# Kernel tuning notes

Measured on AMD Instinct MI355X. Metric: run time of the kernel, lower is better.

## Reference

```python
import jax, jax.numpy as jnp
import numpy as np


def setup_inputs() -> dict:
    key = jax.random.key(0)
    k1, k2, k3, k4 = jax.random.split(key, 4)
    B, N, F, H, O = 4, 2048, 256, 8, 256
    nodes = jax.random.normal(k1, (B, N, F), dtype=jnp.float32)
    W_heads = jax.random.normal(k2, (H, F, F), dtype=jnp.float32) * (1.0 / np.sqrt(F))
    W_out = jax.random.normal(k3, (H * F, O), dtype=jnp.float32) * (1.0 / np.sqrt(H * F))
    bias = jax.random.normal(k4, (O,), dtype=jnp.float32) * 0.02
    return {"nodes": nodes, "W_heads": W_heads, "W_out": W_out, "bias": bias}


def reference(nodes, W_heads, W_out, bias):
    # nodes: [B,N,F]; W_heads: [H,F,F]; W_out: [H*F,O]; bias: [O]
    B, N, F = nodes.shape
    H = W_heads.shape[0]
    norm = 1.0 / jnp.sqrt(jnp.asarray(F, dtype=nodes.dtype))
    # per-head bilinear scores: (x @ W_h) @ x^T  -> [B,H,N,N]
    xw = jnp.einsum('bnf,hfg->bhng', nodes, W_heads)
    scores = jnp.einsum('bhng,bmg->bhnm', xw, nodes) * norm
    att = jax.nn.softmax(scores, axis=-1)
    # messages: att @ x (V = input nodes) -> [B,H,N,F]
    msgs = jnp.einsum('bhnm,bmf->bhnf', att, nodes)
    # concat heads along feature axis (head 0 first) -> [B,N,H*F]
    msgs = msgs.transpose(0, 2, 1, 3).reshape(B, N, H * F)
    return jnp.matmul(msgs, W_out) + bias
```

## Files before the change

### kernel.cpp

```cpp
#include <hip/hip_runtime.h>
#include <hip/hip_bf16.h>

#define B_ 4
#define N_ 2048
#define F_ 256
#define H_ 8
#define O_ 256

#define SCALE_QK 0.09016844005556021f

typedef __attribute__((ext_vector_type(8))) short short8;
typedef __attribute__((ext_vector_type(4))) short s16x4;
typedef __attribute__((ext_vector_type(4))) float f32x4;
typedef __attribute__((ext_vector_type(4))) unsigned int u32x4;

static __device__ __forceinline__ float bf2f(short u) {
    unsigned int x = ((unsigned int)(unsigned short)u) << 16;
    return __builtin_bit_cast(float, x);
}
static __device__ __forceinline__ short f2bf(float f) {
    unsigned int x = __builtin_bit_cast(unsigned int, f);
    unsigned int lsb = (x >> 16) & 1u;
    x += 0x7fffu + lsb;
    return (short)(x >> 16);
}
static __device__ __forceinline__ unsigned int cvtpk(float a, float b) {
    unsigned int r;
    asm("v_cvt_pk_bf16_f32 %0, %1, %2" : "=v"(r) : "v"(a), "v"(b));
    return r;
}

static __device__ __forceinline__ void gld16(const short* g, short* l) {
    __builtin_amdgcn_global_load_lds(
        (const __attribute__((address_space(1))) void*)g,
        (__attribute__((address_space(3))) void*)l, 16, 0, 0);
}

__global__ __launch_bounds__(256) void cvtT_kernel(const float* __restrict__ src,
                                                   short* __restrict__ dstT,
                                                   short* __restrict__ dst2,
                                                   int R, int C) {
    __shared__ short tile[32][33];
    src  += (size_t)blockIdx.z * R * C;
    dstT += (size_t)blockIdx.z * R * C;
    if (dst2) dst2 += (size_t)blockIdx.z * R * C;
    int tx = threadIdx.x, ty = threadIdx.y;
    int c0 = blockIdx.x * 32, r0 = blockIdx.y * 32;
#pragma unroll
    for (int j = 0; j < 4; j++) {
        int r = r0 + ty + j * 8;
        short v = f2bf(src[(size_t)r * C + c0 + tx]);
        tile[ty + j * 8][tx] = v;
        if (dst2) dst2[(size_t)r * C + c0 + tx] = v;
    }
    __syncthreads();
#pragma unroll
    for (int j = 0; j < 4; j++) {
        int c = c0 + ty + j * 8;
        dstT[(size_t)c * R + r0 + tx] = tile[tx][ty + j * 8];
    }
}

__global__ __launch_bounds__(512) void out_kernel(const short* __restrict__ msgs,
                                                  const short* __restrict__ WoutT,
                                                  const float* __restrict__ bias,
                                                  float* __restrict__ out) {
    __shared__ short sA[2][64 * 64];
    __shared__ short sB[2][128 * 64];
    int mt = blockIdx.x, nt = blockIdx.y;
    int tid = threadIdx.x, w = tid >> 6, l = tid & 63, lq = l & 15, quad = l >> 4;
    const short* Arow = msgs  + (size_t)(mt * 64)  * (H_ * F_);
    const short* Brow = WoutT + (size_t)(nt * 128) * (H_ * F_);
    int xk = (l & 7) ^ (l >> 3);

    f32x4 acc[4];
#pragma unroll
    for (int i = 0; i < 4; i++) acc[i] = (f32x4)(0.f);

#define STAGE_OUT(KB, BI) do {                                               \
        gld16(&Arow[(size_t)(w * 8 + (l >> 3)) * (H_ * F_) + (KB) * 64 + xk * 8], \
              &sA[BI][w * 8 * 64]);                                          \
        gld16(&Brow[(size_t)(w * 16 + (l >> 3)) * (H_ * F_) + (KB) * 64 + xk * 8], \
              &sB[BI][w * 16 * 64]);                                         \
        gld16(&Brow[(size_t)(w * 16 + 8 + (l >> 3)) * (H_ * F_) + (KB) * 64 + xk * 8], \
              &sB[BI][(w * 16 + 8) * 64]);                                   \
    } while (0)

    STAGE_OUT(0, 0);
    __syncthreads();

#pragma unroll 1
    for (int kb = 0; kb < 32; kb++) {
        int cur = kb & 1;
        if (kb < 31) STAGE_OUT(kb + 1, cur ^ 1);
        int arow = (w & 3) * 16 + lq;
#pragma unroll
        for (int kk = 0; kk < 2; kk++) {
            short8 af = *(const short8*)&sA[cur][arow * 64 + (((kk * 4 + quad) ^ (arow & 7)) * 8)];
#pragma unroll
            for (int ct = 0; ct < 4; ct++) {
                int brow = (w >> 2) * 64 + ct * 16 + lq;
                short8 bf = *(const short8*)&sB[cur][brow * 64 + (((kk * 4 + quad) ^ (brow & 7)) * 8)];
                acc[ct] = __builtin_amdgcn_mfma_f32_16x16x32_bf16(af, bf, acc[ct], 0, 0, 0);
            }
        }
        __syncthreads();
    }

#pragma unroll
    for (int ct = 0; ct < 4; ct++) {
        int gcol = nt * 128 + (w >> 2) * 64 + ct * 16 + lq;
        float bv = bias[gcol];
#pragma unroll
        for (int r = 0; r < 4; r++) {
            int row = mt * 64 + (w & 3) * 16 + quad * 4 + r;
            out[(size_t)row * O_ + gcol] = acc[ct][r] + bv;
        }
    }
}


#define STAGE_KV(KT, KVF, KVTF) do {                                         \
    _Pragma("unroll")                                                        \
    for (int i_ = 0; i_ < 4; i_++) {                                         \
        int rk_ = w * 8 + i_ * 2 + (l >> 5);                                 \
        int bk_ = (l & 31) ^ (rk_ & 31);                                     \
        gld16(&Xb[(size_t)((KT) * 64 + rk_) * F_ + bk_ * 8],                 \
              &KVF[(w * 8 + i_ * 2) * 256]);                                 \
        int rt_ = w * 32 + i_ * 8 + (l >> 3);                                \
        int bt_ = (l & 7) ^ (rt_ & 7);                                       \
        gld16(&XTb[(size_t)rt_ * N_ + (KT) * 64 + bt_ * 8],                  \
              &KVTF[(w * 32 + i_ * 8) * 64]);                                \
    }                                                                        \
} while (0)

#define COMPUTE_KT(KVF, KVTF) do {                                           \
    f32x4 sacc[4];                                                           \
    _Pragma("unroll")                                                        \
    for (int ct = 0; ct < 4; ct++) sacc[ct] = (f32x4)(0.f);                  \
    __builtin_amdgcn_s_setprio(1);                                           \
    _Pragma("unroll")                                                        \
    for (int kk = 0; kk < 8; kk++) {                                         \
        _Pragma("unroll")                                                    \
        for (int ct = 0; ct < 4; ct++) {                                     \
            int arow = ct * 16 + lq;                                         \
            int ab = (kk * 4 + quad) ^ (arow & 31);                          \
            short8 af = *(const short8*)&KVF[arow * 256 + ab * 8];           \
            sacc[ct] = __builtin_amdgcn_mfma_f32_16x16x32_bf16(af, aq[kk], sacc[ct], 0, 0, 0); \
        }                                                                    \
    }                                                                        \
    __builtin_amdgcn_s_setprio(0);                                           \
    float mx = -INFINITY;                                                    \
    _Pragma("unroll")                                                        \
    for (int ct = 0; ct < 4; ct++)                                           \
        _Pragma("unroll")                                                    \
        for (int r_ = 0; r_ < 4; r_++) mx = fmaxf(mx, sacc[ct][r_]);         \
    mx = fmaxf(mx, __shfl_xor(mx, 16));                                      \
    mx = fmaxf(mx, __shfl_xor(mx, 32));                                      \
    if (!__all(mx - m_q <= 8.0f)) {                \
        float mn = fmaxf(m_q, mx);                                           \
        float alpha = exp2f(m_q - mn);                                       \
        m_q = mn;                                                            \
        l_q *= alpha;                                                        \
        _Pragma("unroll")                                                    \
        for (int ct = 0; ct < 16; ct++)                                      \
            _Pragma("unroll")                                                \
            for (int r_ = 0; r_ < 4; r_++) oacc[ct][r_] *= alpha;            \
    }                                                                        \
    float pv[4][4]; float s_ = 0.f;                                          \
    _Pragma("unroll")                                                        \
    for (int ct = 0; ct < 4; ct++)                                           \
        _Pragma("unroll")                                                    \
        for (int r_ = 0; r_ < 4; r_++) {                                     \
            pv[ct][r_] = exp2f(sacc[ct][r_] - m_q);                          \
            s_ += pv[ct][r_];                                                \
        }                                                                    \
    s_ += __shfl_xor(s_, 16);                                                \
    s_ += __shfl_xor(s_, 32);                                                \
    l_q += s_;                                                               \
    unsigned int w2[4][2];                                                   \
    _Pragma("unroll")                                                        \
    for (int ct = 0; ct < 4; ct++) {                                         \
        w2[ct][0] = cvtpk(pv[ct][0], pv[ct][1]);                             \
        w2[ct][1] = cvtpk(pv[ct][2], pv[ct][3]);                             \
    }                                                                        \
    int sl0 = (2 * (quad & 1)) * 16 + lq;                                    \
    int sl1 = sl0 + 16;                                                      \
    bool hi = (quad >> 1) != 0;                                              \
    short8 pfrag[2];                                                         \
    _Pragma("unroll")                                                        \
    for (int kk = 0; kk < 2; kk++) {                                         \
        unsigned int u0 = __shfl((int)w2[2 * kk][0], sl0);                   \
        unsigned int u1 = __shfl((int)w2[2 * kk][1], sl0);                   \
        unsigned int u2 = __shfl((int)w2[2 * kk][0], sl1);                   \
        unsigned int u3 = __shfl((int)w2[2 * kk][1], sl1);                   \
        unsigned int v0 = __shfl((int)w2[2 * kk + 1][0], sl0);               \
        unsigned int v1 = __shfl((int)w2[2 * kk + 1][1], sl0);               \
        unsigned int v2 = __shfl((int)w2[2 * kk + 1][0], sl1);               \
        unsigned int v3 = __shfl((int)w2[2 * kk + 1][1], sl1);               \
        u32x4 pk = { hi ? v0 : u0, hi ? v1 : u1, hi ? v2 : u2, hi ? v3 : u3 }; \
        pfrag[kk] = __builtin_bit_cast(short8, pk);                          \
    }                                                                        \
    __builtin_amdgcn_s_setprio(1);                                           \
    _Pragma("unroll")                                                        \
    for (int ct = 0; ct < 16; ct++) {                                        \
        int arow = ct * 16 + lq;                                             \
        short8 a0 = *(const short8*)&KVTF[arow * 64 + ((quad) ^ (arow & 7)) * 8]; \
        short8 a1 = *(const short8*)&KVTF[arow * 64 + ((4 + quad) ^ (arow & 7)) * 8]; \
        oacc[ct] = __builtin_amdgcn_mfma_f32_16x16x32_bf16(a0, pfrag[0], oacc[ct], 0, 0, 0); \
        oacc[ct] = __builtin_amdgcn_mfma_f32_16x16x32_bf16(a1, pfrag[1], oacc[ct], 0, 0, 0); \
    }                                                                        \
    __builtin_amdgcn_s_setprio(0);                                           \
} while (0)

__global__ __launch_bounds__(512) void attn_kernel(const short* __restrict__ X,
                                                   const short* __restrict__ WhT,
                                                   const short* __restrict__ XT,
                                                   short* __restrict__ msgs) {
    __shared__ short kvfA[64 * 256];
    __shared__ short kvfB[64 * 256];
    __shared__ short kvTfA[256 * 64];
    __shared__ short kvTfB[256 * 64];

    int qt = blockIdx.x, bh = blockIdx.y, b = bh >> 3, h = bh & 7;
    int tid = threadIdx.x, w = tid >> 6, l = tid & 63, lq = l & 15, quad = l >> 4;
    int q0 = qt * 128;

    const short* Xb  = X  + (size_t)b * N_ * F_;
    const short* XTb = XT + (size_t)b * F_ * N_;
    const short* Whh = WhT + (size_t)h * F_ * F_;

    f32x4 oacc[16];
    short8 aq[8];

#pragma unroll
    for (int i = 0; i < 16; i++) oacc[i] = (f32x4)(0.f);
    {
        short* xdst = (w < 4) ? kvfA : kvfB;
        int wl = w & 3;
#pragma unroll
        for (int i = 0; i < 8; i++) {
            int r = wl * 16 + i * 2 + (l >> 5);
            int bb = (l & 31) ^ (r & 31);
            gld16(&Xb[(size_t)(q0 + ((w >> 2) * 64) + r) * F_ + bb * 8],
                  &xdst[(wl * 16 + i * 2) * 256]);
        }
    }
    const short* xsrc = (w < 4) ? kvfA : kvfB;
#pragma unroll 1
    for (int kb = 0; kb < 4; kb++) {
        __syncthreads();
#pragma unroll
        for (int i = 0; i < 4; i++) {
            int rt = w * 32 + i * 8 + (l >> 3);
            int bt = (l & 7) ^ (rt & 7);
            gld16(&Whh[(size_t)rt * F_ + kb * 64 + bt * 8], &kvTfA[(w * 32 + i * 8) * 64]);
        }
        __syncthreads();
#pragma unroll
        for (int kk = 0; kk < 2; kk++) {
            int arow = (w & 3) * 16 + lq;
            int ab = (kb * 8 + kk * 4 + quad) ^ (arow & 31);
            short8 af = *(const short8*)&xsrc[arow * 256 + ab * 8];
#pragma unroll
            for (int ct = 0; ct < 16; ct++) {
                int brow = ct * 16 + lq;
                int bb = (kk * 4 + quad) ^ (brow & 7);
                short8 bf = *(const short8*)&kvTfA[brow * 64 + bb * 8];
                oacc[ct] = __builtin_amdgcn_mfma_f32_16x16x32_bf16(af, bf, oacc[ct], 0, 0, 0);
            }
        }
    }
    __syncthreads();
    {
        short* qdst = (w < 4) ? kvTfA : kvTfB;
#pragma unroll
        for (int ct = 0; ct < 16; ct++) {
#pragma unroll
            for (int r = 0; r < 4; r++) {
                int row = (w & 3) * 16 + quad * 4 + r;
                int col = ct * 16 + lq;
                int pb = (col >> 3) ^ (row & 31);
                qdst[row * 256 + pb * 8 + (col & 7)] = f2bf(oacc[ct][r] * SCALE_QK);
            }
        }
        __syncthreads();
#pragma unroll
        for (int kk = 0; kk < 8; kk++) {
            int row = (w & 3) * 16 + lq;
            int ab = (kk * 4 + quad) ^ (row & 31);
            aq[kk] = *(const short8*)&qdst[row * 256 + ab * 8];
        }
    }
    __syncthreads();

#pragma unroll
    for (int i = 0; i < 16; i++) oacc[i] = (f32x4)(0.f);
    float m_q = -INFINITY, l_q = 0.f;

    STAGE_KV(0, kvfA, kvTfA);
    __syncthreads();

#pragma unroll 1
    for (int kt2 = 0; kt2 < 16; kt2++) {
        STAGE_KV(2 * kt2 + 1, kvfB, kvTfB);
        COMPUTE_KT(kvfA, kvTfA);
        __syncthreads();
        STAGE_KV((2 * kt2 + 2) & 31, kvfA, kvTfA);
        COMPUTE_KT(kvfB, kvTfB);
        __syncthreads();
    }

    float inv = 1.f / l_q;
    short* Mout = msgs + (size_t)(b * N_ + q0 + w * 16 + lq) * (H_ * F_) + h * F_;
#pragma unroll
    for (int ct = 0; ct < 16; ct++) {
        s16x4 v4 = { f2bf(oacc[ct][0] * inv), f2bf(oacc[ct][1] * inv),
                     f2bf(oacc[ct][2] * inv), f2bf(oacc[ct][3] * inv) };
        *(s16x4*)&Mout[ct * 16 + quad * 4] = v4;
    }
}

extern "C" void kernel_launch(void* const* d_in, const int* in_sizes, int n_in,
                              void* d_out, int out_size, void* d_ws, size_t ws_size,
                              hipStream_t stream) {
    const float* nodes = (const float*)d_in[0];
    const float* Wh    = (const float*)d_in[1];
    const float* Wout  = (const float*)d_in[2];
    const float* bias  = (const float*)d_in[3];
    float* out = (float*)d_out;

    char* ws = (char*)d_ws;
    short* msgs   = (short*)(ws);
    short* WhT    = (short*)(ws + 33554432);
    short* WoutT  = (short*)(ws + 34603008);
    short* XT     = (short*)(ws + 35651584);
    short* Xbf    = (short*)(ws + 39845888);

    dim3 tblk(32, 8, 1);
    hipLaunchKernelGGL(cvtT_kernel, dim3(8, 8, 8),  tblk, 0, stream, Wh,    WhT,   (short*)nullptr, 256,  256);
    hipLaunchKernelGGL(cvtT_kernel, dim3(8, 64, 1), tblk, 0, stream, Wout,  WoutT, (short*)nullptr, 2048, 256);
    hipLaunchKernelGGL(cvtT_kernel, dim3(8, 64, 4), tblk, 0, stream, nodes, XT,    Xbf,             2048, 256);

    hipLaunchKernelGGL(attn_kernel, dim3(16, 32), dim3(512), 0, stream, Xbf, WhT, XT, msgs);
    hipLaunchKernelGGL(out_kernel,  dim3(128, 2), dim3(512), 0, stream, msgs, WoutT, bias, out);
}
```

Measured before the change: 289.0 us.

## Split KV tile across wave pairs, each wave handling two query blocks

Restructures the attention loop so each pair of waves shares 32 query rows. Each wave computes scores for two 16-row query blocks but only against half of each 64-key tile, reusing every K and V fragment loaded from LDS for two MFMAs. Partial softmax states (max and sum) and output accumulators are merged through shared memory at the end. This cuts LDS reads per MFMA and doubles the output accumulator registers, at the cost of a final cross-wave reduction and possibly lower occupancy.

```diff
diff --git a/kernel.cpp b/kernel.cpp
--- a/kernel.cpp
+++ b/kernel.cpp
@@ -135,80 +135,85 @@
 } while (0)
 
 #define COMPUTE_KT(KVF, KVTF) do {                                           \
-    f32x4 sacc[4];                                                           \
-    _Pragma("unroll")                                                        \
-    for (int ct = 0; ct < 4; ct++) sacc[ct] = (f32x4)(0.f);                  \
+    f32x4 sacc[2][2];                                                        \
+    _Pragma("unroll")                                                        \
+    for (int qb = 0; qb < 2; qb++)                                           \
+        _Pragma("unroll")                                                    \
+        for (int ct = 0; ct < 2; ct++) sacc[qb][ct] = (f32x4)(0.f);          \
     __builtin_amdgcn_s_setprio(1);                                           \
     _Pragma("unroll")                                                        \
     for (int kk = 0; kk < 8; kk++) {                                         \
         _Pragma("unroll")                                                    \
-        for (int ct = 0; ct < 4; ct++) {                                     \
-            int arow = ct * 16 + lq;                                         \
+        for (int ct = 0; ct < 2; ct++) {                                     \
+            int arow = KH + ct * 16 + lq;                                    \
             int ab = (kk * 4 + quad) ^ (arow & 31);                          \
             short8 af = *(const short8*)&KVF[arow * 256 + ab * 8];           \
-            sacc[ct] = __builtin_amdgcn_mfma_f32_16x16x32_bf16(af, aq[kk], sacc[ct], 0, 0, 0); \
+            sacc[0][ct] = __builtin_amdgcn_mfma_f32_16x16x32_bf16(af, aq[0][kk], sacc[0][ct], 0, 0, 0); \
+            sacc[1][ct] = __builtin_amdgcn_mfma_f32_16x16x32_bf16(af, aq[1][kk], sacc[1][ct], 0, 0, 0); \
         }                                                                    \
     }                                                                        \
     __builtin_amdgcn_s_setprio(0);                                           \
-    float mx = -INFINITY;                                                    \
-    _Pragma("unroll")                                                        \
-    for (int ct = 0; ct < 4; ct++)                                           \
-        _Pragma("unroll")                                                    \
-        for (int r_ = 0; r_ < 4; r_++) mx = fmaxf(mx, sacc[ct][r_]);         \
-    mx = fmaxf(mx, __shfl_xor(mx, 16));                                      \
-    mx = fmaxf(mx, __shfl_xor(mx, 32));                                      \
-    if (!__all(mx - m_q <= 8.0f)) {                \
-        float mn = fmaxf(m_q, mx);                                           \
-        float alpha = exp2f(m_q - mn);                                       \
-        m_q = mn;                                                            \
-        l_q *= alpha;                                                        \
-        _Pragma("unroll")                                                    \
-        for (int ct = 0; ct < 16; ct++)                                      \
+    unsigned int w2[2][2][2];                                                \
+    _Pragma("unroll")                                                        \
+    for (int qb = 0; qb < 2; qb++) {                                         \
+        float mx = -INFINITY;                                                \
+        _Pragma("unroll")                                                    \
+        for (int ct = 0; ct < 2; ct++)                                       \
             _Pragma("unroll")                                                \
-            for (int r_ = 0; r_ < 4; r_++) oacc[ct][r_] *= alpha;            \
-    }                                                                        \
-    float pv[4][4]; float s_ = 0.f;                                          \
-    _Pragma("unroll")                                                        \
-    for (int ct = 0; ct < 4; ct++)                                           \
-        _Pragma("unroll")                                                    \
-        for (int r_ = 0; r_ < 4; r_++) {                                     \
-            pv[ct][r_] = exp2f(sacc[ct][r_] - m_q);                          \
-            s_ += pv[ct][r_];                                                \
+            for (int r_ = 0; r_ < 4; r_++) mx = fmaxf(mx, sacc[qb][ct][r_]); \
+        mx = fmaxf(mx, __shfl_xor(mx, 16));                                  \
+        mx = fmaxf(mx, __shfl_xor(mx, 32));                                  \
+        if (!__all(mx - m_q[qb] <= 8.0f)) {               \
+            float mn = fmaxf(m_q[qb], mx);                                   \
+            float alpha = exp2f(m_q[qb] - mn);                               \
+            m_q[qb] = mn;                                                    \
+            l_q[qb] *= alpha;                                                \
+            _Pragma("unroll")                                                \
+            for (int ct = 0; ct < 16; ct++)                                  \
+                _Pragma("unroll")                                            \
+                for (int r_ = 0; r_ < 4; r_++) oacc[qb][ct][r_] *= alpha;    \
         }                                                                    \
-    s_ += __shfl_xor(s_, 16);                                                \
-    s_ += __shfl_xor(s_, 32);                                                \
-    l_q += s_;                                                               \
-    unsigned int w2[4][2];                                                   \
-    _Pragma("unroll")                                                        \
-    for (int ct = 0; ct < 4; ct++) {                                         \
-        w2[ct][0] = cvtpk(pv[ct][0], pv[ct][1]);                             \
-        w2[ct][1] = cvtpk(pv[ct][2], pv[ct][3]);                             \
+        float pv[2][4]; float s_ = 0.f;                                      \
+        _Pragma("unroll")                                                    \
+        for (int ct = 0; ct < 2; ct++)                                       \
+            _Pragma("unroll")                                                \
+            for (int r_ = 0; r_ < 4; r_++) {                                 \
+                pv[ct][r_] = exp2f(sacc[qb][ct][r_] - m_q[qb]);              \
+                s_ += pv[ct][r_];                                            \
+            }                                                                \
+        s_ += __shfl_xor(s_, 16);                                            \
+        s_ += __shfl_xor(s_, 32);                                            \
+        l_q[qb] += s_;                                                       \
+        _Pragma("unroll")                                                    \
+        for (int ct = 0; ct < 2; ct++) {                                     \
+            w2[qb][ct][0] = cvtpk(pv[ct][0], pv[ct][1]);                     \
+            w2[qb][ct][1] = cvtpk(pv[ct][2], pv[ct][3]);                     \
+        }                                                                    \
     }                                                                        \
     int sl0 = (2 * (quad & 1)) * 16 + lq;                                    \
     int sl1 = sl0 + 16;                                                      \
     bool hi = (quad >> 1) != 0;                                              \
     short8 pfrag[2];                                                         \
     _Pragma("unroll")                                                        \
-    for (int kk = 0; kk < 2; kk++) {                                         \
-        unsigned int u0 = __shfl((int)w2[2 * kk][0], sl0);                   \
-        unsigned int u1 = __shfl((int)w2[2 * kk][1], sl0);                   \
-        unsigned int u2 = __shfl((int)w2[2 * kk][0], sl1);                   \
-        unsigned int u3 = __shfl((int)w2[2 * kk][1], sl1);                   \
-        unsigned int v0 = __shfl((int)w2[2 * kk + 1][0], sl0);               \
-        unsigned int v1 = __shfl((int)w2[2 * kk + 1][1], sl0);               \
-        unsigned int v2 = __shfl((int)w2[2 * kk + 1][0], sl1);               \
-        unsigned int v3 = __shfl((int)w2[2 * kk + 1][1], sl1);               \
+    for (int qb = 0; qb < 2; qb++) {                                         \
+        unsigned int u0 = __shfl((int)w2[qb][0][0], sl0);                    \
+        unsigned int u1 = __shfl((int)w2[qb][0][1], sl0);                    \
+        unsigned int u2 = __shfl((int)w2[qb][0][0], sl1);                    \
+        unsigned int u3 = __shfl((int)w2[qb][0][1], sl1);                    \
+        unsigned int v0 = __shfl((int)w2[qb][1][0], sl0);                    \
+        unsigned int v1 = __shfl((int)w2[qb][1][1], sl0);                    \
+        unsigned int v2 = __shfl((int)w2[qb][1][0], sl1);                    \
+        unsigned int v3 = __shfl((int)w2[qb][1][1], sl1);                    \
         u32x4 pk = { hi ? v0 : u0, hi ? v1 : u1, hi ? v2 : u2, hi ? v3 : u3 }; \
-        pfrag[kk] = __builtin_bit_cast(short8, pk);                          \
+        pfrag[qb] = __builtin_bit_cast(short8, pk);                          \
     }                                                                        \
     __builtin_amdgcn_s_setprio(1);                                           \
     _Pragma("unroll")                                                        \
     for (int ct = 0; ct < 16; ct++) {                                        \
         int arow = ct * 16 + lq;                                             \
-        short8 a0 = *(const short8*)&KVTF[arow * 64 + ((quad) ^ (arow & 7)) * 8]; \
-        short8 a1 = *(const short8*)&KVTF[arow * 64 + ((4 + quad) ^ (arow & 7)) * 8]; \
-        oacc[ct] = __builtin_amdgcn_mfma_f32_16x16x32_bf16(a0, pfrag[0], oacc[ct], 0, 0, 0); \
-        oacc[ct] = __builtin_amdgcn_mfma_f32_16x16x32_bf16(a1, pfrag[1], oacc[ct], 0, 0, 0); \
+        short8 a0 = *(const short8*)&KVTF[arow * 64 + (((KH4 + quad) ^ (arow & 7)) * 8)]; \
+        oacc[0][ct] = __builtin_amdgcn_mfma_f32_16x16x32_bf16(a0, pfrag[0], oacc[0][ct], 0, 0, 0); \
+        oacc[1][ct] = __builtin_amdgcn_mfma_f32_16x16x32_bf16(a0, pfrag[1], oacc[1][ct], 0, 0, 0); \
     }                                                                        \
     __builtin_amdgcn_s_setprio(0);                                           \
 } while (0)
@@ -217,24 +222,27 @@
                                                    const short* __restrict__ WhT,
                                                    const short* __restrict__ XT,
                                                    short* __restrict__ msgs) {
-    __shared__ short kvfA[64 * 256];
-    __shared__ short kvfB[64 * 256];
-    __shared__ short kvTfA[256 * 64];
-    __shared__ short kvTfB[256 * 64];
+    __shared__ __attribute__((aligned(16))) short kvfA[64 * 256];
+    __shared__ __attribute__((aligned(16))) short kvfB[64 * 256];
+    __shared__ __attribute__((aligned(16))) short kvTfA[256 * 64];
+    __shared__ __attribute__((aligned(16))) short kvTfB[256 * 64];
+    __shared__ float mbuf[8][2][16];
+    __shared__ float lbuf[8][2][16];
 
     int qt = blockIdx.x, bh = blockIdx.y, b = bh >> 3, h = bh & 7;
     int tid = threadIdx.x, w = tid >> 6, l = tid & 63, lq = l & 15, quad = l >> 4;
     int q0 = qt * 128;
+    int KH = (w & 1) * 32, KH4 = (w & 1) * 4;
 
     const short* Xb  = X  + (size_t)b * N_ * F_;
     const short* XTb = XT + (size_t)b * F_ * N_;
     const short* Whh = WhT + (size_t)h * F_ * F_;
 
-    f32x4 oacc[16];
-    short8 aq[8];
-
-#pragma unroll
-    for (int i = 0; i < 16; i++) oacc[i] = (f32x4)(0.f);
+    f32x4 oacc[2][16];
+    short8 aq[2][8];
+
+#pragma unroll
+    for (int i = 0; i < 16; i++) oacc[0][i] = (f32x4)(0.f);
     {
         short* xdst = (w < 4) ? kvfA : kvfB;
         int wl = w & 3;
@@ -267,7 +275,7 @@
                 int brow = ct * 16 + lq;
                 int bb = (kk * 4 + quad) ^ (brow & 7);
                 short8 bf = *(const short8*)&kvTfA[brow * 64 + bb * 8];
-                oacc[ct] = __builtin_amdgcn_mfma_f32_16x16x32_bf16(af, bf, oacc[ct], 0, 0, 0);
+                oacc[0][ct] = __builtin_amdgcn_mfma_f32_16x16x32_bf16(af, bf, oacc[0][ct], 0, 0, 0);
             }
         }
     }
@@ -281,22 +289,28 @@
                 int row = (w & 3) * 16 + quad * 4 + r;
                 int col = ct * 16 + lq;
                 int pb = (col >> 3) ^ (row & 31);
-                qdst[row * 256 + pb * 8 + (col & 7)] = f2bf(oacc[ct][r] * SCALE_QK);
-            }
-        }
-        __syncthreads();
-#pragma unroll
-        for (int kk = 0; kk < 8; kk++) {
-            int row = (w & 3) * 16 + lq;
-            int ab = (kk * 4 + quad) ^ (row & 31);
-            aq[kk] = *(const short8*)&qdst[row * 256 + ab * 8];
-        }
-    }
-    __syncthreads();
-
-#pragma unroll
-    for (int i = 0; i < 16; i++) oacc[i] = (f32x4)(0.f);
-    float m_q = -INFINITY, l_q = 0.f;
+                qdst[row * 256 + pb * 8 + (col & 7)] = f2bf(oacc[0][ct][r] * SCALE_QK);
+            }
+        }
+        __syncthreads();
+        const short* qsrc = (w < 4) ? kvTfA : kvTfB;
+#pragma unroll
+        for (int qb = 0; qb < 2; qb++) {
+#pragma unroll
+            for (int kk = 0; kk < 8; kk++) {
+                int row = ((w >> 1) & 1) * 32 + qb * 16 + lq;
+                int ab = (kk * 4 + quad) ^ (row & 31);
+                aq[qb][kk] = *(const short8*)&qsrc[row * 256 + ab * 8];
+            }
+        }
+    }
+    __syncthreads();
+
+#pragma unroll
+    for (int qb = 0; qb < 2; qb++)
+#pragma unroll
+        for (int i = 0; i < 16; i++) oacc[qb][i] = (f32x4)(0.f);
+    float m_q[2] = { -INFINITY, -INFINITY }, l_q[2] = { 0.f, 0.f };
 
     STAGE_KV(0, kvfA, kvTfA);
     __syncthreads();
@@ -311,13 +325,50 @@
         __syncthreads();
     }
 
-    float inv = 1.f / l_q;
-    short* Mout = msgs + (size_t)(b * N_ + q0 + w * 16 + lq) * (H_ * F_) + h * F_;
-#pragma unroll
-    for (int ct = 0; ct < 16; ct++) {
-        s16x4 v4 = { f2bf(oacc[ct][0] * inv), f2bf(oacc[ct][1] * inv),
-                     f2bf(oacc[ct][2] * inv), f2bf(oacc[ct][3] * inv) };
-        *(s16x4*)&Mout[ct * 16 + quad * 4] = v4;
+#pragma unroll
+    for (int qb = 0; qb < 2; qb++) {
+        mbuf[w][qb][lq] = m_q[qb];
+        lbuf[w][qb][lq] = l_q[qb];
+    }
+    __syncthreads();
+    float a_own[2], inv[2];
+#pragma unroll
+    for (int qb = 0; qb < 2; qb++) {
+        float mp = mbuf[w ^ 1][qb][lq], lp = lbuf[w ^ 1][qb][lq];
+        float mm = fmaxf(m_q[qb], mp);
+        float ao = exp2f(m_q[qb] - mm), ap = exp2f(mp - mm);
+        a_own[qb] = ao;
+        inv[qb] = 1.f / (l_q[qb] * ao + lp * ap);
+    }
+    int pr = w >> 1;
+    float* obuf = (float*)(pr == 0 ? (void*)kvfA : pr == 1 ? (void*)kvfB
+                           : pr == 2 ? (void*)kvTfA : (void*)kvTfB);
+    if (!(w & 1)) {
+#pragma unroll
+        for (int qb = 0; qb < 2; qb++)
+#pragma unroll
+            for (int ct = 0; ct < 16; ct++) {
+                int word = (qb * 16 + lq) * 256 + ((ct * 16 + quad * 4) ^ ((lq & 7) * 4));
+                f32x4 v = oacc[qb][ct] * a_own[qb];
+                *(f32x4*)&obuf[word] = v;
+            }
+    }
+    __syncthreads();
+    if (w & 1) {
+        short* Mout = msgs + (size_t)(b * N_ + q0 + pr * 32 + lq) * (H_ * F_) + h * F_;
+#pragma unroll
+        for (int qb = 0; qb < 2; qb++) {
+#pragma unroll
+            for (int ct = 0; ct < 16; ct++) {
+                int word = (qb * 16 + lq) * 256 + ((ct * 16 + quad * 4) ^ ((lq & 7) * 4));
+                f32x4 o = *(const f32x4*)&obuf[word];
+                s16x4 v4;
+#pragma unroll
+                for (int r = 0; r < 4; r++)
+                    v4[r] = f2bf((o[r] + oacc[qb][ct][r] * a_own[qb]) * inv[qb]);
+                *(s16x4*)&Mout[(size_t)qb * 16 * (H_ * F_) + ct * 16 + quad * 4] = v4;
+            }
+        }
     }
 }
 
```

After: 454.0 us. 57.1% more time.

## Merge conversion launches and double-buffer W_head tiles in attention projection

Applied to the files above, without the earlier changes.

Folds the three transpose/convert launches into a single prep kernel that dispatches on block index, removing two kernel launches. In the attention kernel's Q-projection loop, the next W_head k-slice is now prefetched into an alternate LDS buffer while MFMAs run on the current one, replacing two barriers per iteration with one. Correctness depends on kvTfB being free during this phase, since it is reused later.

```diff
diff --git a/kernel.cpp b/kernel.cpp
--- a/kernel.cpp
+++ b/kernel.cpp
@@ -36,16 +36,33 @@
         (__attribute__((address_space(3))) void*)l, 16, 0, 0);
 }
 
-__global__ __launch_bounds__(256) void cvtT_kernel(const float* __restrict__ src,
-                                                   short* __restrict__ dstT,
-                                                   short* __restrict__ dst2,
-                                                   int R, int C) {
+__global__ __launch_bounds__(256) void prep_kernel(const float* __restrict__ nodes,
+                                                   const float* __restrict__ Wh,
+                                                   const float* __restrict__ Wout,
+                                                   short* __restrict__ Xbf,
+                                                   short* __restrict__ XT,
+                                                   short* __restrict__ WhT,
+                                                   short* __restrict__ WoutT) {
     __shared__ short tile[32][33];
-    src  += (size_t)blockIdx.z * R * C;
-    dstT += (size_t)blockIdx.z * R * C;
-    if (dst2) dst2 += (size_t)blockIdx.z * R * C;
+    int id = blockIdx.x;
+    const float* src; short* dstT; short* dst2; int R, C, bx, by;
+    if (id < 512) {
+        int z = id >> 6, rem = id & 63;
+        src = Wh + (size_t)z * 65536; dstT = WhT + (size_t)z * 65536; dst2 = nullptr;
+        R = 256; C = 256; bx = rem & 7; by = rem >> 3;
+    } else if (id < 1024) {
+        int rem = id - 512;
+        src = Wout; dstT = WoutT; dst2 = nullptr;
+        R = 2048; C = 256; bx = rem & 7; by = rem >> 3;
+    } else {
+        int rem = id - 1024;
+        int z = rem >> 9; rem &= 511;
+        src = nodes + (size_t)z * 524288; dstT = XT + (size_t)z * 524288;
+        dst2 = Xbf + (size_t)z * 524288;
+        R = 2048; C = 256; bx = rem & 7; by = rem >> 3;
+    }
     int tx = threadIdx.x, ty = threadIdx.y;
-    int c0 = blockIdx.x * 32, r0 = blockIdx.y * 32;
+    int c0 = bx * 32, r0 = by * 32;
 #pragma unroll
     for (int j = 0; j < 4; j++) {
         int r = r0 + ty + j * 8;
@@ -246,17 +263,29 @@
                   &xdst[(wl * 16 + i * 2) * 256]);
         }
     }
-    const short* xsrc = (w < 4) ? kvfA : kvfB;
-#pragma unroll 1
-    for (int kb = 0; kb < 4; kb++) {
-        __syncthreads();
+    {
 #pragma unroll
         for (int i = 0; i < 4; i++) {
             int rt = w * 32 + i * 8 + (l >> 3);
             int bt = (l & 7) ^ (rt & 7);
-            gld16(&Whh[(size_t)rt * F_ + kb * 64 + bt * 8], &kvTfA[(w * 32 + i * 8) * 64]);
-        }
-        __syncthreads();
+            gld16(&Whh[(size_t)rt * F_ + bt * 8], &kvTfA[(w * 32 + i * 8) * 64]);
+        }
+    }
+    const short* xsrc = (w < 4) ? kvfA : kvfB;
+    __syncthreads();
+#pragma unroll 1
+    for (int kb = 0; kb < 4; kb++) {
+        short* wnext = (kb & 1) ? kvTfA : kvTfB;
+        const short* wsrc = (kb & 1) ? kvTfB : kvTfA;
+        if (kb < 3) {
+#pragma unroll
+            for (int i = 0; i < 4; i++) {
+                int rt = w * 32 + i * 8 + (l >> 3);
+                int bt = (l & 7) ^ (rt & 7);
+                gld16(&Whh[(size_t)rt * F_ + (kb + 1) * 64 + bt * 8],
+                      &wnext[(w * 32 + i * 8) * 64]);
+            }
+        }
 #pragma unroll
         for (int kk = 0; kk < 2; kk++) {
             int arow = (w & 3) * 16 + lq;
@@ -266,12 +295,12 @@
             for (int ct = 0; ct < 16; ct++) {
                 int brow = ct * 16 + lq;
                 int bb = (kk * 4 + quad) ^ (brow & 7);
-                short8 bf = *(const short8*)&kvTfA[brow * 64 + bb * 8];
+                short8 bf = *(const short8*)&wsrc[brow * 64 + bb * 8];
                 oacc[ct] = __builtin_amdgcn_mfma_f32_16x16x32_bf16(af, bf, oacc[ct], 0, 0, 0);
             }
         }
-    }
-    __syncthreads();
+        __syncthreads();
+    }
     {
         short* qdst = (w < 4) ? kvTfA : kvTfB;
 #pragma unroll
@@ -337,11 +366,8 @@
     short* XT     = (short*)(ws + 35651584);
     short* Xbf    = (short*)(ws + 39845888);
 
-    dim3 tblk(32, 8, 1);
-    hipLaunchKernelGGL(cvtT_kernel, dim3(8, 8, 8),  tblk, 0, stream, Wh,    WhT,   (short*)nullptr, 256,  256);
-    hipLaunchKernelGGL(cvtT_kernel, dim3(8, 64, 1), tblk, 0, stream, Wout,  WoutT, (short*)nullptr, 2048, 256);
-    hipLaunchKernelGGL(cvtT_kernel, dim3(8, 64, 4), tblk, 0, stream, nodes, XT,    Xbf,             2048, 256);
-
+    hipLaunchKernelGGL(prep_kernel, dim3(3072), dim3(32, 8), 0, stream,
+                       nodes, Wh, Wout, Xbf, XT, WhT, WoutT);
     hipLaunchKernelGGL(attn_kernel, dim3(16, 32), dim3(512), 0, stream, Xbf, WhT, XT, msgs);
     hipLaunchKernelGGL(out_kernel,  dim3(128, 2), dim3(512), 0, stream, msgs, WoutT, bias, out);
 }
```

Measured after the change: 294.9 us. +2.1%, slower.

## Process two query groups per wave in attention kernel with 4-wave blocks

Applied to the files above, without the earlier changes.

Each attention block now runs 4 waves instead of 8, and each wave handles two 16-row query groups. Every K/V fragment read from LDS feeds two MFMAs, which halves LDS read traffic per unit of math. The cost is roughly double the accumulator registers per wave (two 16-tile output accumulators plus two query fragment sets) and fewer waves per block to hide latency. Launch bounds are set to one block per SM-equivalent so the compiler can use more registers.

```diff
diff --git a/kernel.cpp b/kernel.cpp
--- a/kernel.cpp
+++ b/kernel.cpp
@@ -122,22 +122,24 @@
 
 #define STAGE_KV(KT, KVF, KVTF) do {                                         \
     _Pragma("unroll")                                                        \
-    for (int i_ = 0; i_ < 4; i_++) {                                         \
-        int rk_ = w * 8 + i_ * 2 + (l >> 5);                                 \
+    for (int i_ = 0; i_ < 8; i_++) {                                         \
+        int rk_ = w * 16 + i_ * 2 + (l >> 5);                                \
         int bk_ = (l & 31) ^ (rk_ & 31);                                     \
         gld16(&Xb[(size_t)((KT) * 64 + rk_) * F_ + bk_ * 8],                 \
-              &KVF[(w * 8 + i_ * 2) * 256]);                                 \
-        int rt_ = w * 32 + i_ * 8 + (l >> 3);                                \
+              &KVF[(w * 16 + i_ * 2) * 256]);                                \
+        int rt_ = w * 64 + i_ * 8 + (l >> 3);                                \
         int bt_ = (l & 7) ^ (rt_ & 7);                                       \
         gld16(&XTb[(size_t)rt_ * N_ + (KT) * 64 + bt_ * 8],                  \
-              &KVTF[(w * 32 + i_ * 8) * 64]);                                \
+              &KVTF[(w * 64 + i_ * 8) * 64]);                                \
     }                                                                        \
 } while (0)
 
 #define COMPUTE_KT(KVF, KVTF) do {                                           \
-    f32x4 sacc[4];                                                           \
-    _Pragma("unroll")                                                        \
-    for (int ct = 0; ct < 4; ct++) sacc[ct] = (f32x4)(0.f);                  \
+    f32x4 sacc[2][4];                                                        \
+    _Pragma("unroll")                                                        \
+    for (int qg = 0; qg < 2; qg++)                                           \
+        _Pragma("unroll")                                                    \
+        for (int ct = 0; ct < 4; ct++) sacc[qg][ct] = (f32x4)(0.f);          \
     __builtin_amdgcn_s_setprio(1);                                           \
     _Pragma("unroll")                                                        \
     for (int kk = 0; kk < 8; kk++) {                                         \
@@ -146,60 +148,64 @@
             int arow = ct * 16 + lq;                                         \
             int ab = (kk * 4 + quad) ^ (arow & 31);                          \
             short8 af = *(const short8*)&KVF[arow * 256 + ab * 8];           \
-            sacc[ct] = __builtin_amdgcn_mfma_f32_16x16x32_bf16(af, aq[kk], sacc[ct], 0, 0, 0); \
+            sacc[0][ct] = __builtin_amdgcn_mfma_f32_16x16x32_bf16(af, aq[0][kk], sacc[0][ct], 0, 0, 0); \
+            sacc[1][ct] = __builtin_amdgcn_mfma_f32_16x16x32_bf16(af, aq[1][kk], sacc[1][ct], 0, 0, 0); \
         }                                                                    \
     }                                                                        \
     __builtin_amdgcn_s_setprio(0);                                           \
-    float mx = -INFINITY;                                                    \
-    _Pragma("unroll")                                                        \
-    for (int ct = 0; ct < 4; ct++)                                           \
-        _Pragma("unroll")                                                    \
-        for (int r_ = 0; r_ < 4; r_++) mx = fmaxf(mx, sacc[ct][r_]);         \
-    mx = fmaxf(mx, __shfl_xor(mx, 16));                                      \
-    mx = fmaxf(mx, __shfl_xor(mx, 32));                                      \
-    if (!__all(mx - m_q <= 8.0f)) {                \
-        float mn = fmaxf(m_q, mx);                                           \
-        float alpha = exp2f(m_q - mn);                                       \
-        m_q = mn;                                                            \
-        l_q *= alpha;                                                        \
-        _Pragma("unroll")                                                    \
-        for (int ct = 0; ct < 16; ct++)                                      \
-            _Pragma("unroll")                                                \
-            for (int r_ = 0; r_ < 4; r_++) oacc[ct][r_] *= alpha;            \
-    }                                                                        \
-    float pv[4][4]; float s_ = 0.f;                                          \
-    _Pragma("unroll")                                                        \
-    for (int ct = 0; ct < 4; ct++)                                           \
-        _Pragma("unroll")                                                    \
-        for (int r_ = 0; r_ < 4; r_++) {                                     \
-            pv[ct][r_] = exp2f(sacc[ct][r_] - m_q);                          \
-            s_ += pv[ct][r_];                                                \
-        }                                                                    \
-    s_ += __shfl_xor(s_, 16);                                                \
-    s_ += __shfl_xor(s_, 32);                                                \
-    l_q += s_;                                                               \
-    unsigned int w2[4][2];                                                   \
-    _Pragma("unroll")                                                        \
-    for (int ct = 0; ct < 4; ct++) {                                         \
-        w2[ct][0] = cvtpk(pv[ct][0], pv[ct][1]);                             \
-        w2[ct][1] = cvtpk(pv[ct][2], pv[ct][3]);                             \
-    }                                                                        \
+    short8 pfrag[2][2];                                                      \
     int sl0 = (2 * (quad & 1)) * 16 + lq;                                    \
     int sl1 = sl0 + 16;                                                      \
     bool hi = (quad >> 1) != 0;                                              \
-    short8 pfrag[2];                                                         \
-    _Pragma("unroll")                                                        \
-    for (int kk = 0; kk < 2; kk++) {                                         \
-        unsigned int u0 = __shfl((int)w2[2 * kk][0], sl0);                   \
-        unsigned int u1 = __shfl((int)w2[2 * kk][1], sl0);                   \
-        unsigned int u2 = __shfl((int)w2[2 * kk][0], sl1);                   \
-        unsigned int u3 = __shfl((int)w2[2 * kk][1], sl1);                   \
-        unsigned int v0 = __shfl((int)w2[2 * kk + 1][0], sl0);               \
-        unsigned int v1 = __shfl((int)w2[2 * kk + 1][1], sl0);               \
-        unsigned int v2 = __shfl((int)w2[2 * kk + 1][0], sl1);               \
-        unsigned int v3 = __shfl((int)w2[2 * kk + 1][1], sl1);               \
-        u32x4 pk = { hi ? v0 : u0, hi ? v1 : u1, hi ? v2 : u2, hi ? v3 : u3 }; \
-        pfrag[kk] = __builtin_bit_cast(short8, pk);                          \
+    _Pragma("unroll")                                                        \
+    for (int qg = 0; qg < 2; qg++) {                                         \
+        float mx = -INFINITY;                                                \
+        _Pragma("unroll")                                                    \
+        for (int ct = 0; ct < 4; ct++)                                       \
+            _Pragma("unroll")                                                \
+            for (int r_ = 0; r_ < 4; r_++) mx = fmaxf(mx, sacc[qg][ct][r_]); \
+        mx = fmaxf(mx, __shfl_xor(mx, 16));                                  \
+        mx = fmaxf(mx, __shfl_xor(mx, 32));                                  \
+        if (!__all(mx - m_q[qg] <= 8.0f)) {        \
+            float mn = fmaxf(m_q[qg], mx);                                   \
+            float alpha = exp2f(m_q[qg] - mn);                               \
+            m_q[qg] = mn;                                                    \
+            l_q[qg] *= alpha;                                                \
+            _Pragma("unroll")                                                \
+            for (int ct = 0; ct < 16; ct++)                                  \
+                _Pragma("unroll")                                            \
+                for (int r_ = 0; r_ < 4; r_++) oacc[qg][ct][r_] *= alpha;    \
+        }                                                                    \
+        float pv[4][4]; float s_ = 0.f;                                      \
+        _Pragma("unroll")                                                    \
+        for (int ct = 0; ct < 4; ct++)                                       \
+            _Pragma("unroll")                                                \
+            for (int r_ = 0; r_ < 4; r_++) {                                 \
+                pv[ct][r_] = exp2f(sacc[qg][ct][r_] - m_q[qg]);              \
+                s_ += pv[ct][r_];                                            \
+            }                                                                \
+        s_ += __shfl_xor(s_, 16);                                            \
+        s_ += __shfl_xor(s_, 32);                                            \
+        l_q[qg] += s_;                                                       \
+        unsigned int w2[4][2];                                               \
+        _Pragma("unroll")                                                    \
+        for (int ct = 0; ct < 4; ct++) {                                     \
+            w2[ct][0] = cvtpk(pv[ct][0], pv[ct][1]);                         \
+            w2[ct][1] = cvtpk(pv[ct][2], pv[ct][3]);                         \
+        }                                                                    \
+        _Pragma("unroll")                                                    \
+        for (int kk = 0; kk < 2; kk++) {                                     \
+            unsigned int u0 = __shfl((int)w2[2 * kk][0], sl0);               \
+            unsigned int u1 = __shfl((int)w2[2 * kk][1], sl0);               \
+            unsigned int u2 = __shfl((int)w2[2 * kk][0], sl1);               \
+            unsigned int u3 = __shfl((int)w2[2 * kk][1], sl1);               \
+            unsigned int v0 = __shfl((int)w2[2 * kk + 1][0], sl0);           \
+            unsigned int v1 = __shfl((int)w2[2 * kk + 1][1], sl0);           \
+            unsigned int v2 = __shfl((int)w2[2 * kk + 1][0], sl1);           \
+            unsigned int v3 = __shfl((int)w2[2 * kk + 1][1], sl1);           \
+            u32x4 pk = { hi ? v0 : u0, hi ? v1 : u1, hi ? v2 : u2, hi ? v3 : u3 }; \
+            pfrag[qg][kk] = __builtin_bit_cast(short8, pk);                  \
+        }                                                                    \
     }                                                                        \
     __builtin_amdgcn_s_setprio(1);                                           \
     _Pragma("unroll")                                                        \
@@ -207,16 +213,18 @@
         int arow = ct * 16 + lq;                                             \
         short8 a0 = *(const short8*)&KVTF[arow * 64 + ((quad) ^ (arow & 7)) * 8]; \
         short8 a1 = *(const short8*)&KVTF[arow * 64 + ((4 + quad) ^ (arow & 7)) * 8]; \
-        oacc[ct] = __builtin_amdgcn_mfma_f32_16x16x32_bf16(a0, pfrag[0], oacc[ct], 0, 0, 0); \
-        oacc[ct] = __builtin_amdgcn_mfma_f32_16x16x32_bf16(a1, pfrag[1], oacc[ct], 0, 0, 0); \
+        oacc[0][ct] = __builtin_amdgcn_mfma_f32_16x16x32_bf16(a0, pfrag[0][0], oacc[0][ct], 0, 0, 0); \
+        oacc[0][ct] = __builtin_amdgcn_mfma_f32_16x16x32_bf16(a1, pfrag[0][1], oacc[0][ct], 0, 0, 0); \
+        oacc[1][ct] = __builtin_amdgcn_mfma_f32_16x16x32_bf16(a0, pfrag[1][0], oacc[1][ct], 0, 0, 0); \
+        oacc[1][ct] = __builtin_amdgcn_mfma_f32_16x16x32_bf16(a1, pfrag[1][1], oacc[1][ct], 0, 0, 0); \
     }                                                                        \
     __builtin_amdgcn_s_setprio(0);                                           \
 } while (0)
 
-__global__ __launch_bounds__(512) void attn_kernel(const short* __restrict__ X,
-                                                   const short* __restrict__ WhT,
-                                                   const short* __restrict__ XT,
-                                                   short* __restrict__ msgs) {
+__global__ __launch_bounds__(256, 1) void attn_kernel(const short* __restrict__ X,
+                                                      const short* __restrict__ WhT,
+                                                      const short* __restrict__ XT,
+                                                      short* __restrict__ msgs) {
     __shared__ short kvfA[64 * 256];
     __shared__ short kvfB[64 * 256];
     __shared__ short kvTfA[256 * 64];
@@ -230,73 +238,84 @@
     const short* XTb = XT + (size_t)b * F_ * N_;
     const short* Whh = WhT + (size_t)h * F_ * F_;
 
-    f32x4 oacc[16];
-    short8 aq[8];
-
-#pragma unroll
-    for (int i = 0; i < 16; i++) oacc[i] = (f32x4)(0.f);
+    f32x4 oacc[2][16];
+    short8 aq[2][8];
+
+#pragma unroll
+    for (int qg = 0; qg < 2; qg++)
+#pragma unroll
+        for (int i = 0; i < 16; i++) oacc[qg][i] = (f32x4)(0.f);
     {
-        short* xdst = (w < 4) ? kvfA : kvfB;
-        int wl = w & 3;
-#pragma unroll
-        for (int i = 0; i < 8; i++) {
-            int r = wl * 16 + i * 2 + (l >> 5);
+        short* xdst = (w < 2) ? kvfA : kvfB;
+        int wl = w & 1;
+#pragma unroll
+        for (int i = 0; i < 16; i++) {
+            int r = wl * 32 + i * 2 + (l >> 5);
             int bb = (l & 31) ^ (r & 31);
-            gld16(&Xb[(size_t)(q0 + ((w >> 2) * 64) + r) * F_ + bb * 8],
-                  &xdst[(wl * 16 + i * 2) * 256]);
-        }
-    }
-    const short* xsrc = (w < 4) ? kvfA : kvfB;
+            gld16(&Xb[(size_t)(q0 + ((w >> 1) * 64) + r) * F_ + bb * 8],
+                  &xdst[(wl * 32 + i * 2) * 256]);
+        }
+    }
+    const short* xsrc = (w < 2) ? kvfA : kvfB;
 #pragma unroll 1
     for (int kb = 0; kb < 4; kb++) {
         __syncthreads();
 #pragma unroll
-        for (int i = 0; i < 4; i++) {
-            int rt = w * 32 + i * 8 + (l >> 3);
+        for (int i = 0; i < 8; i++) {
+            int rt = w * 64 + i * 8 + (l >> 3);
             int bt = (l & 7) ^ (rt & 7);
-            gld16(&Whh[(size_t)rt * F_ + kb * 64 + bt * 8], &kvTfA[(w * 32 + i * 8) * 64]);
+            gld16(&Whh[(size_t)rt * F_ + kb * 64 + bt * 8], &kvTfA[(w * 64 + i * 8) * 64]);
         }
         __syncthreads();
 #pragma unroll
         for (int kk = 0; kk < 2; kk++) {
-            int arow = (w & 3) * 16 + lq;
-            int ab = (kb * 8 + kk * 4 + quad) ^ (arow & 31);
-            short8 af = *(const short8*)&xsrc[arow * 256 + ab * 8];
+#pragma unroll
+            for (int qg = 0; qg < 2; qg++) {
+                int arow = (w & 1) * 32 + qg * 16 + lq;
+                int ab = (kb * 8 + kk * 4 + quad) ^ (arow & 31);
+                short8 af = *(const short8*)&xsrc[arow * 256 + ab * 8];
+#pragma unroll
+                for (int ct = 0; ct < 16; ct++) {
+                    int brow = ct * 16 + lq;
+                    int bb = (kk * 4 + quad) ^ (brow & 7);
+                    short8 bf = *(const short8*)&kvTfA[brow * 64 + bb * 8];
+                    oacc[qg][ct] = __builtin_amdgcn_mfma_f32_16x16x32_bf16(af, bf, oacc[qg][ct], 0, 0, 0);
+                }
+            }
+        }
+    }
+    __syncthreads();
+    {
+        short* qdst = (w < 2) ? kvTfA : kvTfB;
+#pragma unroll
+        for (int qg = 0; qg < 2; qg++)
 #pragma unroll
             for (int ct = 0; ct < 16; ct++) {
-                int brow = ct * 16 + lq;
-                int bb = (kk * 4 + quad) ^ (brow & 7);
-                short8 bf = *(const short8*)&kvTfA[brow * 64 + bb * 8];
-                oacc[ct] = __builtin_amdgcn_mfma_f32_16x16x32_bf16(af, bf, oacc[ct], 0, 0, 0);
+#pragma unroll
+                for (int r = 0; r < 4; r++) {
+                    int row = (w & 1) * 32 + qg * 16 + quad * 4 + r;
+                    int col = ct * 16 + lq;
+                    int pb = (col >> 3) ^ (row & 31);
+                    qdst[row * 256 + pb * 8 + (col & 7)] = f2bf(oacc[qg][ct][r] * SCALE_QK);
+                }
             }
-        }
-    }
-    __syncthreads();
-    {
-        short* qdst = (w < 4) ? kvTfA : kvTfB;
-#pragma unroll
-        for (int ct = 0; ct < 16; ct++) {
-#pragma unroll
-            for (int r = 0; r < 4; r++) {
-                int row = (w & 3) * 16 + quad * 4 + r;
-                int col = ct * 16 + lq;
-                int pb = (col >> 3) ^ (row & 31);
-                qdst[row * 256 + pb * 8 + (col & 7)] = f2bf(oacc[ct][r] * SCALE_QK);
+        __syncthreads();
+#pragma unroll
+        for (int qg = 0; qg < 2; qg++)
+#pragma unroll
+            for (int kk = 0; kk < 8; kk++) {
+                int row = (w & 1) * 32 + qg * 16 + lq;
+                int ab = (kk * 4 + quad) ^ (row & 31);
+                aq[qg][kk] = *(const short8*)&qdst[row * 256 + ab * 8];
             }
-        }
-        __syncthreads();
-#pragma unroll
-        for (int kk = 0; kk < 8; kk++) {
-            int row = (w & 3) * 16 + lq;
-            int ab = (kk * 4 + quad) ^ (row & 31);
-            aq[kk] = *(const short8*)&qdst[row * 256 + ab * 8];
-        }
-    }
-    __syncthreads();
-
-#pragma unroll
-    for (int i = 0; i < 16; i++) oacc[i] = (f32x4)(0.f);
-    float m_q = -INFINITY, l_q = 0.f;
+    }
+    __syncthreads();
+
+#pragma unroll
+    for (int qg = 0; qg < 2; qg++)
+#pragma unroll
+        for (int i = 0; i < 16; i++) oacc[qg][i] = (f32x4)(0.f);
+    float m_q[2] = { -INFINITY, -INFINITY }, l_q[2] = { 0.f, 0.f };
 
     STAGE_KV(0, kvfA, kvTfA);
     __syncthreads();
@@ -311,13 +330,16 @@
         __syncthreads();
     }
 
-    float inv = 1.f / l_q;
-    short* Mout = msgs + (size_t)(b * N_ + q0 + w * 16 + lq) * (H_ * F_) + h * F_;
-#pragma unroll
-    for (int ct = 0; ct < 16; ct++) {
-        s16x4 v4 = { f2bf(oacc[ct][0] * inv), f2bf(oacc[ct][1] * inv),
-                     f2bf(oacc[ct][2] * inv), f2bf(oacc[ct][3] * inv) };
-        *(s16x4*)&Mout[ct * 16 + quad * 4] = v4;
+#pragma unroll
+    for (int qg = 0; qg < 2; qg++) {
+        float inv = 1.f / l_q[qg];
+        short* Mout = msgs + (size_t)(b * N_ + q0 + w * 32 + qg * 16 + lq) * (H_ * F_) + h * F_;
+#pragma unroll
+        for (int ct = 0; ct < 16; ct++) {
+            s16x4 v4 = { f2bf(oacc[qg][ct][0] * inv), f2bf(oacc[qg][ct][1] * inv),
+                         f2bf(oacc[qg][ct][2] * inv), f2bf(oacc[qg][ct][3] * inv) };
+            *(s16x4*)&Mout[ct * 16 + quad * 4] = v4;
+        }
     }
 }
 
@@ -342,6 +364,6 @@
     hipLaunchKernelGGL(cvtT_kernel, dim3(8, 64, 1), tblk, 0, stream, Wout,  WoutT, (short*)nullptr, 2048, 256);
     hipLaunchKernelGGL(cvtT_kernel, dim3(8, 64, 4), tblk, 0, stream, nodes, XT,    Xbf,             2048, 256);
 
-    hipLaunchKernelGGL(attn_kernel, dim3(16, 32), dim3(512), 0, stream, Xbf, WhT, XT, msgs);
+    hipLaunchKernelGGL(attn_kernel, dim3(16, 32), dim3(256), 0, stream, Xbf, WhT, XT, msgs);
     hipLaunchKernelGGL(out_kernel,  dim3(128, 2), dim3(512), 0, stream, msgs, WoutT, bias, out);
 }
```

Measured after the change: 361.2 us. 25.0% more time.
